# Performance work log

Hardware: AMD Instinct MI355X
Metric: run time of the kernel (lower is better)

Reference implementation:

```python
import jax, jax.numpy as jnp
import numpy as np
import itertools

B, H, W, C = 64, 28, 28, 576
NH, WS = 18, 7
KD = C // NH          # head dim = 32 (attn_ratio=1 so d == key_dim)
HID = 4 * C           # mlp hidden
N = WS * WS           # tokens per window = 49


def _bias_idxs():
    points = list(itertools.product(range(WS), range(WS)))
    offsets, idxs = {}, []
    for p1 in points:
        for p2 in points:
            off = (abs(p1[0] - p2[0]), abs(p1[1] - p2[1]))
            if off not in offsets:
                offsets[off] = len(offsets)
            idxs.append(offsets[off])
    return np.asarray(idxs, dtype=np.int64).reshape(N, N), len(offsets)


def setup_inputs() -> dict:
    key = jax.random.key(0)
    ks = jax.random.split(key, 10)
    idxs, n_off = _bias_idxs()  # n_off == 49
    s = 0.02
    return {
        "x": jax.random.normal(ks[0], (B, H * W, C), jnp.float32),
        "gamma_a": jnp.ones((C,), jnp.float32),
        "beta_a": jnp.zeros((C,), jnp.float32),
        "qkv_w": jax.random.normal(ks[1], (3 * C, C), jnp.float32) * s,
        "qkv_b": jnp.zeros((3 * C,), jnp.float32),
        "proj_w": jax.random.normal(ks[2], (C, C), jnp.float32) * s,
        "proj_b": jnp.zeros((C,), jnp.float32),
        "attn_biases": jax.random.normal(ks[3], (NH, n_off), jnp.float32) * s,
        "conv_w": jax.random.normal(ks[4], (C, 1, 3, 3), jnp.float32) * 0.1,
        "bn_gamma": jnp.ones((C,), jnp.float32),
        "bn_beta": jnp.zeros((C,), jnp.float32),
        "bn_mean": jnp.zeros((C,), jnp.float32),
        "bn_var": jax.random.uniform(ks[5], (C,), jnp.float32, 0.5, 1.5),
        "gamma_m": jnp.ones((C,), jnp.float32),
        "beta_m": jnp.zeros((C,), jnp.float32),
        "fc1_w": jax.random.normal(ks[6], (HID, C), jnp.float32) * s,
        "fc1_b": jnp.zeros((HID,), jnp.float32),
        "fc2_w": jax.random.normal(ks[7], (C, HID), jnp.float32) * s,
        "fc2_b": jnp.zeros((C,), jnp.float32),
        "bias_idxs": jnp.asarray(idxs),
    }


def _ln(x, g, b, eps=1e-5):
    mu = x.mean(-1, keepdims=True)
    var = ((x - mu) ** 2).mean(-1, keepdims=True)
    return (x - mu) * jax.lax.rsqrt(var + eps) * g + b


def reference(x, gamma_a, beta_a, qkv_w, qkv_b, proj_w, proj_b, attn_biases,
              conv_w, bn_gamma, bn_beta, bn_mean, bn_var,
              gamma_m, beta_m, fc1_w, fc1_b, fc2_w, fc2_b, bias_idxs):
    scale = KD ** -0.5
    nWh, nWw = H // WS, W // WS
    res = x
    # ---- window partition: (B, H*W, C) -> (B*nWh*nWw, 49, C) ----
    xw = x.reshape(B, nWh, WS, nWw, WS, C).transpose(0, 1, 3, 2, 4, 5)
    xw = xw.reshape(-1, N, C)
    # ---- windowed attention with gathered relative-position bias ----
    h = _ln(xw, gamma_a, beta_a)
    qkv = h @ qkv_w.T + qkv_b                       # (Bw, N, 3C)
    qkv = qkv.reshape(-1, N, NH, 3 * KD)
    q, k, v = jnp.split(qkv, 3, axis=-1)            # each (Bw, N, NH, KD)
    q = q.transpose(0, 2, 1, 3)
    k = k.transpose(0, 2, 1, 3)
    v = v.transpose(0, 2, 1, 3)
    bias = attn_biases[:, bias_idxs]                # (NH, N, N)
    attn = jnp.einsum('bhnd,bhmd->bhnm', q, k) * scale + bias
    attn = jax.nn.softmax(attn, axis=-1)
    out = jnp.einsum('bhnm,bhmd->bhnd', attn, v)    # (Bw, NH, N, KD)
    out = out.transpose(0, 2, 1, 3).reshape(-1, N, C) @ proj_w.T + proj_b
    # ---- window reverse ----
    out = out.reshape(B, nWh, nWw, WS, WS, C).transpose(0, 1, 3, 2, 4, 5)
    out = out.reshape(B, H * W, C)
    x = res + out
    # ---- depthwise 3x3 conv + BatchNorm (inference stats) ----
    xc = x.transpose(0, 2, 1).reshape(B, C, H, W)
    xc = jax.lax.conv_general_dilated(
        xc, conv_w, (1, 1), [(1, 1), (1, 1)],
        feature_group_count=C,
        dimension_numbers=('NCHW', 'OIHW', 'NCHW'))
    eps = 1e-5
    inv = (jax.lax.rsqrt(bn_var + eps) * bn_gamma)[:, None, None]
    xc = (xc - bn_mean[:, None, None]) * inv + bn_beta[:, None, None]
    x = xc.reshape(B, C, H * W).transpose(0, 2, 1)
    # ---- MLP with pre-LayerNorm ----
    hm = _ln(x, gamma_m, beta_m)
    hm = jax.nn.gelu(hm @ fc1_w.T + fc1_b, approximate=False)
    hm = hm @ fc2_w.T + fc2_b
    return x + hm
```

## Files before the change

kernel.cpp:

```cpp
#include <hip/hip_runtime.h>
#include <hip/hip_bf16.h>

typedef __bf16 v8bf  __attribute__((ext_vector_type(8)));
typedef __bf16 v4bf  __attribute__((ext_vector_type(4)));
typedef float  f32x4 __attribute__((ext_vector_type(4)));
typedef float  f32x8 __attribute__((ext_vector_type(8)));

#define TOKENS 50176
#define CDIM   576
#define NHEAD  18
#define QKVD   1728

__device__ __forceinline__ void gld16(const __bf16* g, __bf16* l)
{
    __builtin_amdgcn_global_load_lds(
        (const __attribute__((address_space(1))) void*)g,
        (__attribute__((address_space(3))) void*)l,
        16, 0, 0);
}

__global__ __launch_bounds__(256)
void cast_kernel(const float* __restrict__ in, __bf16* __restrict__ out)
{
    const size_t i = ((size_t)blockIdx.x * 256 + threadIdx.x) * 4;
    f32x4 v = *(const f32x4*)&in[i];
    v4bf o;
#pragma unroll
    for (int j = 0; j < 4; ++j) o[j] = (__bf16)v[j];
    *(v4bf*)&out[i] = o;
}

__global__ __launch_bounds__(64)
void conv_prep(const float* __restrict__ w, const float* __restrict__ bg,
               const float* __restrict__ bb, const float* __restrict__ bm,
               const float* __restrict__ bv, __bf16* __restrict__ wt,
               float* __restrict__ bias2)
{
    const int c = blockIdx.x * 64 + threadIdx.x;
    const float inv = rsqrtf(bv[c] + 1e-5f) * bg[c];
#pragma unroll
    for (int t = 0; t < 9; ++t) wt[t * CDIM + c] = (__bf16)(w[c * 9 + t] * inv);
    bias2[c] = bb[c] - bm[c] * inv;
}

template<typename InT>
__global__ __launch_bounds__(256)
void ln_kernel(const InT* __restrict__ x, const float* __restrict__ g,
               const float* __restrict__ b, __bf16* __restrict__ out)
{
    const int lane = threadIdx.x & 63;
    const int wid  = threadIdx.x >> 6;
    const size_t t = (size_t)blockIdx.x * 4 + wid;
    const InT* row = x + t * CDIM;

    float v[16];
    float sum = 0.f, sq = 0.f;
    if constexpr (sizeof(InT) == 2) {
        v8bf d0 = *(const v8bf*)&row[(size_t)lane * 8];
#pragma unroll
        for (int j = 0; j < 8; ++j) { float f = (float)d0[j]; v[j] = f; sum += f; sq += f * f; }
    } else {
        f32x8 d0 = *(const f32x8*)&row[(size_t)lane * 8];
#pragma unroll
        for (int j = 0; j < 8; ++j) { float f = d0[j]; v[j] = f; sum += f; sq += f * f; }
    }
    if (lane < 8) {
        if constexpr (sizeof(InT) == 2) {
            v8bf d1 = *(const v8bf*)&row[(size_t)(lane + 64) * 8];
#pragma unroll
            for (int j = 0; j < 8; ++j) { float f = (float)d1[j]; v[8 + j] = f; sum += f; sq += f * f; }
        } else {
            f32x8 d1 = *(const f32x8*)&row[(size_t)(lane + 64) * 8];
#pragma unroll
            for (int j = 0; j < 8; ++j) { float f = d1[j]; v[8 + j] = f; sum += f; sq += f * f; }
        }
    }
#pragma unroll
    for (int o = 32; o >= 1; o >>= 1) {
        sum += __shfl_xor(sum, o, 64);
        sq  += __shfl_xor(sq,  o, 64);
    }
    const float mean = sum * (1.0f / CDIM);
    const float rstd = rsqrtf(sq * (1.0f / CDIM) - mean * mean + 1e-5f);

    {
        int c0 = lane * 8;
        v8bf o0;
#pragma unroll
        for (int j = 0; j < 8; ++j)
            o0[j] = (__bf16)((v[j] - mean) * rstd * g[c0 + j] + b[c0 + j]);
        *(v8bf*)&out[t * CDIM + c0] = o0;
    }
    if (lane < 8) {
        int c0 = (lane + 64) * 8;
        v8bf o1;
#pragma unroll
        for (int j = 0; j < 8; ++j)
            o1[j] = (__bf16)((v[8 + j] - mean) * rstd * g[c0 + j] + b[c0 + j]);
        *(v8bf*)&out[t * CDIM + c0] = o1;
    }
}

template<int EPI, typename OutT, typename AddT>
__global__ __launch_bounds__(512, 2)
void gemm_bt(const __bf16* __restrict__ A, const __bf16* __restrict__ W,
             const float* __restrict__ bias, const AddT* __restrict__ add,
             OutT* __restrict__ C, int N, int K, int nN)
{
    constexpr int BM = 256, BN = 128, BK = 64;
    __shared__ __bf16 As[3][BM * BK];
    __shared__ __bf16 Ws[3][BN * BK];
    const int tid = threadIdx.x, lane = tid & 63, wid = tid >> 6;
    const int lr = lane & 15, kh = lane >> 4;
    const int wm = wid >> 1, wn = wid & 1;

    const int nwg = gridDim.x, bid = blockIdx.x;
    const int q = nwg >> 3, r = nwg & 7;
    const int xcd = bid & 7, jj = bid >> 3;
    const int wgid = (xcd < r ? xcd * (q + 1) : r * (q + 1) + (xcd - r) * q) + jj;
    const int mblk = wgid / nN, nblk = wgid - mblk * nN;
    const int m0 = mblk * BM, n0 = nblk * BN;

    const __bf16* pA = A + (size_t)(m0 + wid * 32 + lr) * K + kh * 8;
    const int wrow = min(n0 + wid * 16 + lr, N - 1);
    const __bf16* pW = W + (size_t)wrow * K + kh * 8;

    auto stage = [&](int s, int kt) {
        const int kk = kt * BK;
#pragma unroll
        for (int i = 0; i < 4; ++i)
            gld16(pA + (size_t)((i >> 1) * 16) * K + kk + (i & 1) * 32,
                  &As[s][wid * 2048 + i * 512]);
#pragma unroll
        for (int i = 0; i < 2; ++i)
            gld16(pW + kk + i * 32, &Ws[s][wid * 1024 + i * 512]);
    };

    f32x4 acc[4][4] = {};
    const int nk = K / BK;

    stage(0, 0);
    stage(1, 1);

    for (int t = 0; t < nk; ++t) {
        if (t < nk - 1) asm volatile("s_waitcnt vmcnt(6)" ::: "memory");
        else            asm volatile("s_waitcnt vmcnt(0)" ::: "memory");
        __builtin_amdgcn_s_barrier();
        __builtin_amdgcn_sched_barrier(0);

        const __bf16* as = As[t % 3];
        const __bf16* ws2 = Ws[t % 3];
        v8bf a[2][4], b[2][4];
#pragma unroll
        for (int ks = 0; ks < 2; ++ks) {
            const int ko = (ks * 4 + kh) * 16 + lr;
#pragma unroll
            for (int m = 0; m < 4; ++m)
                a[ks][m] = *(const v8bf*)&as[((wm * 4 + m) * 128 + ko) * 8];
#pragma unroll
            for (int n = 0; n < 4; ++n)
                b[ks][n] = *(const v8bf*)&ws2[((wn * 4 + n) * 128 + ko) * 8];
        }

        if (t + 2 < nk) stage((t + 2) % 3, t + 2);

        __builtin_amdgcn_s_setprio(1);
#pragma unroll
        for (int ks = 0; ks < 2; ++ks)
#pragma unroll
            for (int m = 0; m < 4; ++m)
#pragma unroll
                for (int n = 0; n < 4; ++n)
                    acc[m][n] = __builtin_amdgcn_mfma_f32_16x16x32_bf16(
                        a[ks][m], b[ks][n], acc[m][n], 0, 0, 0);
        __builtin_amdgcn_s_setprio(0);
    }

#pragma unroll
    for (int m = 0; m < 4; ++m)
#pragma unroll
        for (int n = 0; n < 4; ++n)
#pragma unroll
            for (int rr = 0; rr < 4; ++rr) {
                int row = m0 + wm * 64 + m * 16 + kh * 4 + rr;
                int col = n0 + wn * 64 + n * 16 + lr;
                if (col < N) {
                    float vv = acc[m][n][rr] + bias[col];
                    if (EPI == 1) vv += (float)add[(size_t)row * N + col];
                    if (EPI == 2) vv = 0.5f * vv * (1.0f + erff(vv * 0.70710678118654752f));
                    C[(size_t)row * N + col] = (OutT)vv;
                }
            }
}

__global__ __launch_bounds__(64)
void attn_kernel(const __bf16* __restrict__ qkv, const float* __restrict__ biases,
                 const int* __restrict__ bidx, __bf16* __restrict__ out)
{
    const int head = blockIdx.x;
    const int win  = blockIdx.y;
    const int tid  = threadIdx.x;
    const int b  = win >> 4;
    const int wy = (win >> 2) & 3;
    const int wx = win & 3;
    __shared__ float kk[49][32];
    __shared__ float vv[49][32];
    const size_t hb = (size_t)head * 96;

    for (int e = tid; e < 49 * 32; e += 64) {
        int n = e >> 5, d = e & 31;
        int iy = n / 7, ix = n - iy * 7;
        size_t t = (size_t)b * 784 + (size_t)(wy * 7 + iy) * 28 + wx * 7 + ix;
        const __bf16* p = qkv + t * QKVD + hb;
        kk[n][d] = (float)p[32 + d];
        vv[n][d] = (float)p[64 + d];
    }
    float q[32];
    size_t tmine = 0;
    if (tid < 49) {
        int iy = tid / 7, ix = tid - iy * 7;
        tmine = (size_t)b * 784 + (size_t)(wy * 7 + iy) * 28 + wx * 7 + ix;
        const __bf16* p = qkv + tmine * QKVD + hb;
#pragma unroll
        for (int d = 0; d < 32; ++d) q[d] = (float)p[d];
    }
    __syncthreads();
    if (tid >= 49) return;

    const float scale = 0.17677669529663687f;
    float s[49];
    float mx = -1e30f;
    const int*   brow = bidx + tid * 49;
    const float* bh   = biases + head * 49;
#pragma unroll
    for (int m = 0; m < 49; ++m) {
        float dot = 0.f;
#pragma unroll
        for (int d = 0; d < 32; ++d) dot += q[d] * kk[m][d];
        float val = dot * scale + bh[brow[m]];
        s[m] = val;
        mx = fmaxf(mx, val);
    }
    float sum = 0.f;
#pragma unroll
    for (int m = 0; m < 49; ++m) { float e = __expf(s[m] - mx); s[m] = e; sum += e; }
    const float rs = 1.0f / sum;

    __bf16* op = out + tmine * CDIM + (size_t)head * 32;
#pragma unroll
    for (int d = 0; d < 32; ++d) {
        float a = 0.f;
#pragma unroll
        for (int m = 0; m < 49; ++m) a += s[m] * vv[m][d];
        op[d] = (__bf16)(a * rs);
    }
}

__global__ __launch_bounds__(256)
void conv_bn_v(const __bf16* __restrict__ xin, const __bf16* __restrict__ wt,
               const float* __restrict__ bias2, __bf16* __restrict__ xout)
{
    const size_t gt = (size_t)blockIdx.x * 256 + threadIdx.x;
    const int g = (int)(gt % 72);
    const size_t p = gt / 72;
    const int bimg = (int)(p / 784);
    const int pix  = (int)(p - (size_t)bimg * 784);
    const int y = pix / 28, xx = pix - y * 28;
    const int c0 = g * 8;

    float acc[8];
    {
        f32x4 b0 = *(const f32x4*)&bias2[c0];
        f32x4 b1 = *(const f32x4*)&bias2[c0 + 4];
#pragma unroll
        for (int jj = 0; jj < 4; ++jj) { acc[jj] = b0[jj]; acc[4 + jj] = b1[jj]; }
    }
#pragma unroll
    for (int dy = 0; dy < 3; ++dy) {
        int ny = y + dy - 1;
        if (ny < 0 || ny >= 28) continue;
#pragma unroll
        for (int dx = 0; dx < 3; ++dx) {
            int nx = xx + dx - 1;
            if (nx < 0 || nx >= 28) continue;
            v8bf xv = *(const v8bf*)&xin[((size_t)bimg * 784 + ny * 28 + nx) * CDIM + c0];
            v8bf wv = *(const v8bf*)&wt[(dy * 3 + dx) * CDIM + c0];
#pragma unroll
            for (int jj = 0; jj < 8; ++jj) acc[jj] += (float)xv[jj] * (float)wv[jj];
        }
    }
    v8bf o;
#pragma unroll
    for (int jj = 0; jj < 8; ++jj) o[jj] = (__bf16)acc[jj];
    *(v8bf*)&xout[p * CDIM + c0] = o;
}

extern "C" void kernel_launch(void* const* d_in, const int* in_sizes, int n_in,
                              void* d_out, int out_size, void* d_ws, size_t ws_size,
                              hipStream_t stream)
{
    (void)in_sizes; (void)n_in; (void)out_size; (void)ws_size;
    const float* x          = (const float*)d_in[0];
    const float* gamma_a    = (const float*)d_in[1];
    const float* beta_a     = (const float*)d_in[2];
    const float* qkv_w      = (const float*)d_in[3];
    const float* qkv_b      = (const float*)d_in[4];
    const float* proj_w     = (const float*)d_in[5];
    const float* proj_b     = (const float*)d_in[6];
    const float* attn_bias  = (const float*)d_in[7];
    const float* conv_w     = (const float*)d_in[8];
    const float* bn_g       = (const float*)d_in[9];
    const float* bn_b       = (const float*)d_in[10];
    const float* bn_m       = (const float*)d_in[11];
    const float* bn_v       = (const float*)d_in[12];
    const float* gamma_m    = (const float*)d_in[13];
    const float* beta_m     = (const float*)d_in[14];
    const float* fc1_w      = (const float*)d_in[15];
    const float* fc1_b      = (const float*)d_in[16];
    const float* fc2_w      = (const float*)d_in[17];
    const float* fc2_b      = (const float*)d_in[18];
    const int*   bidx       = (const int*)d_in[19];

    const size_t T = TOKENS;
    __bf16* ws     = (__bf16*)d_ws;
    __bf16* hbuf   = ws;
    __bf16* qkvbuf = ws + T * 576;
    __bf16* aout   = ws;
    __bf16* x2     = ws + T * 2304;
    __bf16* x3     = x2 + T * 576;
    __bf16* lnm    = x2;
    __bf16* f1     = ws;
    __bf16* wq     = x3 + T * 576;
    __bf16* wp     = wq + (size_t)QKVD * CDIM;
    __bf16* w1     = wp + (size_t)CDIM * CDIM;
    __bf16* w2     = w1 + (size_t)2304 * CDIM;
    __bf16* wt     = w2 + (size_t)CDIM * 2304;
    float*  bias2  = (float*)(wt + 9 * CDIM);
    float*  outp   = (float*)d_out;

    cast_kernel<<<dim3((QKVD * CDIM) / 1024), 256, 0, stream>>>(qkv_w, wq);
    cast_kernel<<<dim3((CDIM * CDIM) / 1024), 256, 0, stream>>>(proj_w, wp);
    cast_kernel<<<dim3((2304 * CDIM) / 1024), 256, 0, stream>>>(fc1_w, w1);
    cast_kernel<<<dim3((CDIM * 2304) / 1024), 256, 0, stream>>>(fc2_w, w2);
    conv_prep<<<dim3(9), 64, 0, stream>>>(conv_w, bn_g, bn_b, bn_m, bn_v, wt, bias2);

    ln_kernel<float><<<dim3(T / 4), 256, 0, stream>>>(x, gamma_a, beta_a, hbuf);
    gemm_bt<0, __bf16, float><<<dim3(196 * 14), 512, 0, stream>>>(
        hbuf, wq, qkv_b, nullptr, qkvbuf, QKVD, CDIM, 14);
    attn_kernel<<<dim3(NHEAD, 1024), 64, 0, stream>>>(qkvbuf, attn_bias, bidx, aout);
    gemm_bt<1, __bf16, float><<<dim3(196 * 5), 512, 0, stream>>>(
        aout, wp, proj_b, x, x2, CDIM, CDIM, 5);
    conv_bn_v<<<dim3(14112), 256, 0, stream>>>(x2, wt, bias2, x3);
    ln_kernel<__bf16><<<dim3(T / 4), 256, 0, stream>>>(x3, gamma_m, beta_m, lnm);
    gemm_bt<2, __bf16, float><<<dim3(196 * 18), 512, 0, stream>>>(
        lnm, w1, fc1_b, nullptr, f1, 2304, CDIM, 18);
    gemm_bt<1, float, __bf16><<<dim3(196 * 5), 512, 0, stream>>>(
        f1, w2, fc2_b, x3, outp, CDIM, 2304, 5);
}
```

Measured before the change: 1.116 ms.

## Shrink GEMM tile to 128x128, double-buffer LDS, stage epilogue through shared memory

The GEMM block tile shrinks from 256x128 with 8 waves to 128x128 with 4 waves. The three-stage LDS pipeline with explicit vmcnt waits becomes a simpler double buffer synchronised with __syncthreads. The epilogue now writes accumulators to LDS, and each lane then reads back a contiguous 32-column row segment. This allows vectorised bias, residual and GELU processing and 16-byte global stores instead of scattered scalar stores. Costs: less latency hiding from the shallower pipeline, more blocks and extra LDS round trips in the epilogue.

```diff
diff --git a/kernel.cpp b/kernel.cpp
--- a/kernel.cpp
+++ b/kernel.cpp
@@ -102,67 +102,72 @@
 }
 
 template<int EPI, typename OutT, typename AddT>
-__global__ __launch_bounds__(512, 2)
+__global__ __launch_bounds__(256, 2)
 void gemm_bt(const __bf16* __restrict__ A, const __bf16* __restrict__ W,
              const float* __restrict__ bias, const AddT* __restrict__ add,
              OutT* __restrict__ C, int N, int K, int nN)
 {
-    constexpr int BM = 256, BN = 128, BK = 64;
-    __shared__ __bf16 As[3][BM * BK];
-    __shared__ __bf16 Ws[3][BN * BK];
+    constexpr int BM = 128, BN = 128, BK = 64;
+    __shared__ __align__(16) __bf16 LDSBUF[2][(BM + BN) * BK];
     const int tid = threadIdx.x, lane = tid & 63, wid = tid >> 6;
     const int lr = lane & 15, kh = lane >> 4;
     const int wm = wid >> 1, wn = wid & 1;
 
     const int nwg = gridDim.x, bid = blockIdx.x;
     const int q = nwg >> 3, r = nwg & 7;
-    const int xcd = bid & 7, jj = bid >> 3;
-    const int wgid = (xcd < r ? xcd * (q + 1) : r * (q + 1) + (xcd - r) * q) + jj;
+    const int xcd = bid & 7, jc = bid >> 3;
+    const int wgid = (xcd < r ? xcd * (q + 1) : r * (q + 1) + (xcd - r) * q) + jc;
     const int mblk = wgid / nN, nblk = wgid - mblk * nN;
     const int m0 = mblk * BM, n0 = nblk * BN;
 
     const __bf16* pA = A + (size_t)(m0 + wid * 32 + lr) * K + kh * 8;
-    const int wrow = min(n0 + wid * 16 + lr, N - 1);
-    const __bf16* pW = W + (size_t)wrow * K + kh * 8;
+    const int wr0 = min(n0 + wid * 32 + lr, N - 1);
+    const int wr1 = min(n0 + wid * 32 + 16 + lr, N - 1);
+    const __bf16* pW0 = W + (size_t)wr0 * K + kh * 8;
+    const __bf16* pW1 = W + (size_t)wr1 * K + kh * 8;
+
+    const int off = (kh * 16 + lr) * 8;
+
+    f32x4 acc[4][4] = {};
+    const int nk = K / BK;
 
     auto stage = [&](int s, int kt) {
         const int kk = kt * BK;
-#pragma unroll
-        for (int i = 0; i < 4; ++i)
-            gld16(pA + (size_t)((i >> 1) * 16) * K + kk + (i & 1) * 32,
-                  &As[s][wid * 2048 + i * 512]);
+        __bf16* as = &LDSBUF[s][0];
+        __bf16* wsd = &LDSBUF[s][BM * BK];
 #pragma unroll
         for (int i = 0; i < 2; ++i)
-            gld16(pW + kk + i * 32, &Ws[s][wid * 1024 + i * 512]);
+#pragma unroll
+            for (int h = 0; h < 2; ++h)
+                gld16(pA + (size_t)(i * 16) * K + kk + h * 32,
+                      as + wid * 2048 + (i * 2 + h) * 512);
+#pragma unroll
+        for (int h = 0; h < 2; ++h) {
+            gld16(pW0 + kk + h * 32, wsd + wid * 2048 + h * 512);
+            gld16(pW1 + kk + h * 32, wsd + wid * 2048 + (2 + h) * 512);
+        }
     };
 
-    f32x4 acc[4][4] = {};
-    const int nk = K / BK;
-
     stage(0, 0);
-    stage(1, 1);
-
+    int cur = 0;
     for (int t = 0; t < nk; ++t) {
-        if (t < nk - 1) asm volatile("s_waitcnt vmcnt(6)" ::: "memory");
-        else            asm volatile("s_waitcnt vmcnt(0)" ::: "memory");
-        __builtin_amdgcn_s_barrier();
-        __builtin_amdgcn_sched_barrier(0);
-
-        const __bf16* as = As[t % 3];
-        const __bf16* ws2 = Ws[t % 3];
+        __syncthreads();
+        const __bf16* as = &LDSBUF[cur][0];
+        const __bf16* wsrc = &LDSBUF[cur][BM * BK];
         v8bf a[2][4], b[2][4];
 #pragma unroll
         for (int ks = 0; ks < 2; ++ks) {
-            const int ko = (ks * 4 + kh) * 16 + lr;
 #pragma unroll
             for (int m = 0; m < 4; ++m)
-                a[ks][m] = *(const v8bf*)&as[((wm * 4 + m) * 128 + ko) * 8];
+                a[ks][m] = *(const v8bf*)&as[(wm * 2 + (m >> 1)) * 2048 +
+                                             ((m & 1) * 2 + ks) * 512 + off];
 #pragma unroll
             for (int n = 0; n < 4; ++n)
-                b[ks][n] = *(const v8bf*)&ws2[((wn * 4 + n) * 128 + ko) * 8];
-        }
-
-        if (t + 2 < nk) stage((t + 2) % 3, t + 2);
+                b[ks][n] = *(const v8bf*)&wsrc[(wn * 2 + (n >> 1)) * 2048 +
+                                               ((n & 1) * 2 + ks) * 512 + off];
+        }
+
+        if (t + 1 < nk) stage(cur ^ 1, t + 1);
 
         __builtin_amdgcn_s_setprio(1);
 #pragma unroll
@@ -174,23 +179,85 @@
                     acc[m][n] = __builtin_amdgcn_mfma_f32_16x16x32_bf16(
                         a[ks][m], b[ks][n], acc[m][n], 0, 0, 0);
         __builtin_amdgcn_s_setprio(0);
-    }
-
-#pragma unroll
-    for (int m = 0; m < 4; ++m)
-#pragma unroll
-        for (int n = 0; n < 4; ++n)
-#pragma unroll
-            for (int rr = 0; rr < 4; ++rr) {
-                int row = m0 + wm * 64 + m * 16 + kh * 4 + rr;
-                int col = n0 + wn * 64 + n * 16 + lr;
-                if (col < N) {
-                    float vv = acc[m][n][rr] + bias[col];
-                    if (EPI == 1) vv += (float)add[(size_t)row * N + col];
-                    if (EPI == 2) vv = 0.5f * vv * (1.0f + erff(vv * 0.70710678118654752f));
-                    C[(size_t)row * N + col] = (OutT)vv;
+        cur ^= 1;
+    }
+
+    __syncthreads();
+    float* sc = (float*)&LDSBUF[0][0] + wid * (32 * 66);
+
+    const int r0 = lane >> 1, ch = lane & 1;
+    const int gcolr = n0 + wn * 64 + ch * 32;
+    const int gcol  = min(gcolr, N - 32);
+    float bc[32];
+#pragma unroll
+    for (int j4 = 0; j4 < 8; ++j4)
+        *(f32x4*)&bc[j4 * 4] = *(const f32x4*)&bias[gcol + j4 * 4];
+
+#pragma unroll
+    for (int hf = 0; hf < 2; ++hf) {
+#pragma unroll
+        for (int m2 = 0; m2 < 2; ++m2)
+#pragma unroll
+            for (int n = 0; n < 4; ++n)
+#pragma unroll
+                for (int rr = 0; rr < 4; ++rr)
+                    sc[(m2 * 16 + kh * 4 + rr) * 66 + n * 16 + lr] =
+                        acc[hf * 2 + m2][n][rr];
+
+        const int grow = m0 + wm * 64 + hf * 32 + r0;
+        float vals[32];
+#pragma unroll
+        for (int j4 = 0; j4 < 8; ++j4)
+            *(f32x4*)&vals[j4 * 4] = *(const f32x4*)&sc[r0 * 66 + ch * 32 + j4 * 4];
+
+#pragma unroll
+        for (int j = 0; j < 32; ++j) vals[j] += bc[j];
+        if (EPI == 1) {
+            if constexpr (sizeof(AddT) == 2) {
+                const __bf16* ap = (const __bf16*)add + (size_t)grow * N + gcol;
+#pragma unroll
+                for (int g = 0; g < 4; ++g) {
+                    v8bf av = *(const v8bf*)&ap[g * 8];
+#pragma unroll
+                    for (int e = 0; e < 8; ++e) vals[g * 8 + e] += (float)av[e];
+                }
+            } else {
+                const float* ap = (const float*)add + (size_t)grow * N + gcol;
+#pragma unroll
+                for (int j4 = 0; j4 < 8; ++j4) {
+                    f32x4 av = *(const f32x4*)&ap[j4 * 4];
+#pragma unroll
+                    for (int e = 0; e < 4; ++e) vals[j4 * 4 + e] += av[e];
                 }
             }
+        }
+        if (EPI == 2) {
+#pragma unroll
+            for (int j = 0; j < 32; ++j)
+                vals[j] = 0.5f * vals[j] * (1.0f + erff(vals[j] * 0.70710678118654752f));
+        }
+
+        if constexpr (sizeof(OutT) == 2) {
+            __bf16* cp = (__bf16*)C + (size_t)grow * N + gcolr;
+#pragma unroll
+            for (int g = 0; g < 4; ++g) {
+                if (gcolr + g * 8 < N) {
+                    v8bf o;
+#pragma unroll
+                    for (int e = 0; e < 8; ++e) o[e] = (__bf16)vals[g * 8 + e];
+                    *(v8bf*)&cp[g * 8] = o;
+                }
+            }
+        } else {
+            float* cp = (float*)C + (size_t)grow * N + gcolr;
+#pragma unroll
+            for (int j4 = 0; j4 < 8; ++j4) {
+                if (gcolr + j4 * 4 < N)
+                    *(f32x4*)&cp[j4 * 4] = *(const f32x4*)&vals[j4 * 4];
+            }
+        }
+        if (hf == 0) __syncthreads();
+    }
 }
 
 __global__ __launch_bounds__(64)
@@ -345,15 +412,15 @@
     conv_prep<<<dim3(9), 64, 0, stream>>>(conv_w, bn_g, bn_b, bn_m, bn_v, wt, bias2);
 
     ln_kernel<float><<<dim3(T / 4), 256, 0, stream>>>(x, gamma_a, beta_a, hbuf);
-    gemm_bt<0, __bf16, float><<<dim3(196 * 14), 512, 0, stream>>>(
+    gemm_bt<0, __bf16, float><<<dim3(392 * 14), 256, 0, stream>>>(
         hbuf, wq, qkv_b, nullptr, qkvbuf, QKVD, CDIM, 14);
     attn_kernel<<<dim3(NHEAD, 1024), 64, 0, stream>>>(qkvbuf, attn_bias, bidx, aout);
-    gemm_bt<1, __bf16, float><<<dim3(196 * 5), 512, 0, stream>>>(
+    gemm_bt<1, __bf16, float><<<dim3(392 * 5), 256, 0, stream>>>(
         aout, wp, proj_b, x, x2, CDIM, CDIM, 5);
     conv_bn_v<<<dim3(14112), 256, 0, stream>>>(x2, wt, bias2, x3);
     ln_kernel<__bf16><<<dim3(T / 4), 256, 0, stream>>>(x3, gamma_m, beta_m, lnm);
-    gemm_bt<2, __bf16, float><<<dim3(196 * 18), 512, 0, stream>>>(
+    gemm_bt<2, __bf16, float><<<dim3(392 * 18), 256, 0, stream>>>(
         lnm, w1, fc1_b, nullptr, f1, 2304, CDIM, 18);
-    gemm_bt<1, float, __bf16><<<dim3(196 * 5), 512, 0, stream>>>(
+    gemm_bt<1, float, __bf16><<<dim3(392 * 5), 256, 0, stream>>>(
         f1, w2, fc2_b, x3, outp, CDIM, 2304, 5);
 }
```

New measurement: 1.244 ms. 1.11x slower.
